# Optimization experiments

Measured on AMD Instinct MI355X. Metric: run time of the kernel, lower is better.

The kernel has to match this reference:

```python
import jax, jax.numpy as jnp
import numpy as np

N_NODES = 21
HID = 32


def _gcn_norm(edge_index, n):
    # GCNConv normalization with added self-loops (improved=False)
    src, dst = edge_index[0], edge_index[1]
    loop = jnp.arange(n, dtype=src.dtype)
    s = jnp.concatenate([src, loop])
    d = jnp.concatenate([dst, loop])
    w = jnp.ones(s.shape[0], dtype=jnp.float32)
    deg = jnp.zeros(n, dtype=jnp.float32).at[d].add(w)
    dinv = jnp.where(deg > 0, deg ** -0.5, 0.0)
    return s, d, dinv[s] * w * dinv[d]


def _gcn(X, W, b, s, d, norm):
    # X: [B,P,N,F] -> [B,P,N,O]; gather along node axis, scatter-add at targets
    XW = X @ W
    msg = XW[:, :, s, :] * norm[None, None, :, None]
    out = jnp.zeros_like(XW[:, :, :1, :]).repeat(XW.shape[2], axis=2)
    out = jnp.zeros(XW.shape, XW.dtype).at[:, :, d, :].add(msg)
    return out + b


def _forward(x, edge_index, W_z, b_z, W_r, b_r, W_h, b_h,
             lz_W, lz_b, lr_W, lr_b, lh_W, lh_b,
             att, l1_W, l1_b, l2_W, l2_b):
    B, N, F, P = x.shape
    X = jnp.transpose(x, (0, 3, 1, 2))  # [B,P,N,F] -- all periods in parallel
    s, d, norm = _gcn_norm(edge_index, N)
    # A3TGCN2 passes H=None for every period -> hidden state is zeros each call
    H = jnp.zeros((B, P, N, HID), x.dtype)
    Z = jax.nn.sigmoid(jnp.concatenate([_gcn(X, W_z, b_z, s, d, norm), H], -1) @ lz_W + lz_b)
    R = jax.nn.sigmoid(jnp.concatenate([_gcn(X, W_r, b_r, s, d, norm), H], -1) @ lr_W + lr_b)
    Ht = jnp.tanh(jnp.concatenate([_gcn(X, W_h, b_h, s, d, norm), H * R], -1) @ lh_W + lh_b)
    Hn = Z * H + (1.0 - Z) * Ht  # [B,P,N,HID]
    probs = jax.nn.softmax(att)
    h = jnp.einsum('p,bpno->bno', probs, Hn)  # attention pooling over periods
    h = jax.nn.relu(h)
    h = h @ l1_W + l1_b            # [B,N,P]
    h = jnp.transpose(h, (0, 2, 1))  # [B,P,N]
    h = h @ l2_W + l2_b            # [B,P,6]
    return jnp.transpose(h, (0, 2, 1))  # [B,6,P]


def setup_inputs() -> dict:
    key = jax.random.key(0)
    ks = jax.random.split(key, 16)
    B, N, F, P = 1024, N_NODES, 3, 64
    x = jax.random.normal(ks[0], (B, N, F, P), jnp.float32)
    edge_index = jax.random.randint(ks[1], (2, 60), 0, N)
    sc = 0.1
    inp = {
        'x': x, 'edge_index': edge_index,
        'W_z': jax.random.normal(ks[2], (F, HID)) * sc, 'b_z': jnp.zeros(HID),
        'W_r': jax.random.normal(ks[3], (F, HID)) * sc, 'b_r': jnp.zeros(HID),
        'W_h': jax.random.normal(ks[4], (F, HID)) * sc, 'b_h': jnp.zeros(HID),
        'lz_W': jax.random.normal(ks[5], (2 * HID, HID)) * sc, 'lz_b': jnp.zeros(HID),
        'lr_W': jax.random.normal(ks[6], (2 * HID, HID)) * sc, 'lr_b': jnp.zeros(HID),
        'lh_W': jax.random.normal(ks[7], (2 * HID, HID)) * sc, 'lh_b': jnp.zeros(HID),
        'att': jax.random.uniform(ks[8], (P,)),
        'l1_W': jax.random.normal(ks[9], (HID, P)) * sc, 'l1_b': jnp.zeros(P),
        'l2_W': jax.random.normal(ks[10], (N, 6)) * sc, 'l2_b': jnp.zeros(6),
    }
    return inp


def reference(x, edge_index, W_z, b_z, W_r, b_r, W_h, b_h,
              lz_W, lz_b, lr_W, lr_b, lh_W, lh_b,
              att, l1_W, l1_b, l2_W, l2_b):
    return _forward(x, edge_index, W_z, b_z, W_r, b_r, W_h, b_h,
                    lz_W, lz_b, lr_W, lr_b, lh_W, lh_b,
                    att, l1_W, l1_b, l2_W, l2_b)
```

## Files before the change

### kernel.cpp

```cpp
#include <hip/hip_runtime.h>

#define NN   21
#define NE   60
#define FD   3
#define HD   32
#define PP   64
#define OUTC 6

__global__ __launch_bounds__(256, 4) void fused_k(
    const float* __restrict__ x,   const int* __restrict__ edge,
    const float* __restrict__ Wz,  const float* __restrict__ bz,
    const float* __restrict__ Wh,  const float* __restrict__ bh,
    const float* __restrict__ lzW, const float* __restrict__ lzb,
    const float* __restrict__ lhW, const float* __restrict__ lhb,
    const float* __restrict__ att,
    const float* __restrict__ l1W, const float* __restrict__ l1b,
    const float* __restrict__ l2W, const float* __restrict__ l2b,
    float* __restrict__ out)
{
    __shared__ __align__(16) float Xs[NN * FD * PP];
    __shared__ __align__(16) float Ys[NN * FD * PP];
    __shared__ float As[NN * NN];
    __shared__ float degS[NN];
    __shared__ float probs[PP];
    __shared__ float Wzp[FD * HD], Whp[FD * HD], bzp[HD], bhp[HD];
    __shared__ float Hs[NN * HD];
    __shared__ float G[OUTC * HD];
    __shared__ float Sc[OUTC];

    const int t = threadIdx.x;
    const int b = blockIdx.x;
    const float* xb = x + (size_t)b * (NN * FD * PP);

    {
        const float4* xb4 = (const float4*)xb;
        float4* Xs4 = (float4*)Xs;
        for (int i = t; i < NN * FD * PP / 4; i += 256) Xs4[i] = xb4[i];

        float4* Ys4 = (float4*)Ys;
        Ys4[t]       = ((const float4*)lzW)[t];
        Ys4[256 + t] = ((const float4*)lhW)[t];
        if (t < 24)                 Ys4[512 + t]        = ((const float4*)Wz)[t];
        else if (t >= 32 && t < 56) Ys4[536 + (t - 32)] = ((const float4*)Wh)[t - 32];

        for (int i = t; i < NN * NN; i += 256) As[i] = 0.f;
        if (t < NN) degS[t] = 1.f;
    }
    __syncthreads();

    if (t < NE) atomicAdd(&degS[edge[NE + t]], 1.f);
    __syncthreads();

    if (t < NN) degS[t] = rsqrtf(degS[t]);
    __syncthreads();

    if (t < NE) {
        int s = edge[t], d = edge[NE + t];
        atomicAdd(&As[d * NN + s], degS[s] * degS[d]);
    }
    if (t >= 192 && t < 192 + NN) {
        int n = t - 192;
        atomicAdd(&As[n * NN + n], degS[n] * degS[n]);
    }
    if (t < FD * HD) {
        int f = t >> 5, o = t & 31;
        const float* lzWs = Ys;
        const float* lhWs = Ys + 1024;
        const float* WzS  = Ys + 2048;
        const float* WhS  = Ys + 2144;
        float az = 0.f, ah = 0.f;
        #pragma unroll
        for (int k = 0; k < HD; ++k) {
            az = fmaf(WzS[f * HD + k], lzWs[k * HD + o], az);
            ah = fmaf(WhS[f * HD + k], lhWs[k * HD + o], ah);
        }
        Wzp[t] = az; Whp[t] = ah;
    } else if (t < FD * HD + HD) {
        int o = t - FD * HD;
        const float* lzWs = Ys;
        const float* lhWs = Ys + 1024;
        float az = lzb[o], ah = lhb[o];
        #pragma unroll
        for (int k = 0; k < HD; ++k) {
            az = fmaf(bz[k], lzWs[k * HD + o], az);
            ah = fmaf(bh[k], lhWs[k * HD + o], ah);
        }
        bzp[o] = az; bhp[o] = ah;
    } else if (t >= 128 && t < 192) {
        int l = t - 128;
        float a = att[l];
        float m = a;
        #pragma unroll
        for (int msk = 32; msk >= 1; msk >>= 1) m = fmaxf(m, __shfl_xor(m, msk, 64));
        float e = __expf(a - m);
        float ssum = e;
        #pragma unroll
        for (int msk = 32; msk >= 1; msk >>= 1) ssum += __shfl_xor(ssum, msk, 64);
        probs[l] = e / ssum;
    }
    __syncthreads();

    {
        float4* Ys4 = (float4*)Ys;
        const float4* Xs4 = (const float4*)Xs;
        for (int i = t; i < NN * FD * PP / 4; i += 256) {
            int p4 = i & 15;
            int fn = i >> 4;
            int f = fn % 3, n = fn / 3;
            const float* Arow = As + n * NN;
            float4 acc = {0.f, 0.f, 0.f, 0.f};
            #pragma unroll
            for (int m = 0; m < NN; ++m) {
                float a = Arow[m];
                float4 xv = Xs4[(m * 3 + f) * 16 + p4];
                acc.x = fmaf(a, xv.x, acc.x);
                acc.y = fmaf(a, xv.y, acc.y);
                acc.z = fmaf(a, xv.z, acc.z);
                acc.w = fmaf(a, xv.w, acc.w);
            }
            Ys4[fn * 16 + p4] = acc;
        }
    }
    __syncthreads();

    {
        float4* ov4 = (float4*)Xs;
        const float4* l1W4 = (const float4*)l1W;
        for (int i = t; i < 512; i += 256) ov4[i] = l1W4[i];
        if (t < 16) ov4[512 + t] = ((const float4*)l1b)[t];
        if (t >= 64 && t < 64 + 126) Xs[2112 + (t - 64)] = l2W[t - 64];
        if (t >= 224 && t < 230) Xs[2238 + (t - 224)] = l2b[t - 224];
    }

    {
        const int o  = t & 31;
        const int ng = t >> 5;
        const float wz0 = Wzp[o], wz1 = Wzp[HD + o], wz2 = Wzp[2 * HD + o];
        const float wh0 = Whp[o], wh1 = Whp[HD + o], wh2 = Whp[2 * HD + o];
        const float bz0 = bzp[o], bh0 = bhp[o];
        for (int n = ng; n < NN; n += 8) {
            const float4* Yn4 = (const float4*)(Ys + n * FD * PP);
            float a0 = 0.f, a1 = 0.f, a2 = 0.f, a3 = 0.f;
            #pragma unroll
            for (int pq = 0; pq < 16; ++pq) {
                float4 y0 = Yn4[pq], y1 = Yn4[16 + pq], y2 = Yn4[32 + pq];
                {
                    float az = fmaf(y2.x, wz2, fmaf(y1.x, wz1, fmaf(y0.x, wz0, bz0)));
                    float ah = fmaf(y2.x, wh2, fmaf(y1.x, wh1, fmaf(y0.x, wh0, bh0)));
                    float w  = __builtin_amdgcn_rcpf(1.f + __expf(az));
                    float r  = __builtin_amdgcn_rcpf(1.f + __expf(2.f * ah));
                    float ht = fmaf(-2.f, r, 1.f);
                    a0 = fmaf(probs[4 * pq + 0] * w, ht, a0);
                }
                {
                    float az = fmaf(y2.y, wz2, fmaf(y1.y, wz1, fmaf(y0.y, wz0, bz0)));
                    float ah = fmaf(y2.y, wh2, fmaf(y1.y, wh1, fmaf(y0.y, wh0, bh0)));
                    float w  = __builtin_amdgcn_rcpf(1.f + __expf(az));
                    float r  = __builtin_amdgcn_rcpf(1.f + __expf(2.f * ah));
                    float ht = fmaf(-2.f, r, 1.f);
                    a1 = fmaf(probs[4 * pq + 1] * w, ht, a1);
                }
                {
                    float az = fmaf(y2.z, wz2, fmaf(y1.z, wz1, fmaf(y0.z, wz0, bz0)));
                    float ah = fmaf(y2.z, wh2, fmaf(y1.z, wh1, fmaf(y0.z, wh0, bh0)));
                    float w  = __builtin_amdgcn_rcpf(1.f + __expf(az));
                    float r  = __builtin_amdgcn_rcpf(1.f + __expf(2.f * ah));
                    float ht = fmaf(-2.f, r, 1.f);
                    a2 = fmaf(probs[4 * pq + 2] * w, ht, a2);
                }
                {
                    float az = fmaf(y2.w, wz2, fmaf(y1.w, wz1, fmaf(y0.w, wz0, bz0)));
                    float ah = fmaf(y2.w, wh2, fmaf(y1.w, wh1, fmaf(y0.w, wh0, bh0)));
                    float w  = __builtin_amdgcn_rcpf(1.f + __expf(az));
                    float r  = __builtin_amdgcn_rcpf(1.f + __expf(2.f * ah));
                    float ht = fmaf(-2.f, r, 1.f);
                    a3 = fmaf(probs[4 * pq + 3] * w, ht, a3);
                }
            }
            Hs[n * HD + o] = fmaxf((a0 + a1) + (a2 + a3), 0.f);
        }
    }
    __syncthreads();

    {
        const float* l2Ws = Xs + 2112;
        if (t < OUTC * HD) {
            int c = t >> 5, o = t & 31;
            float g = 0.f;
            #pragma unroll
            for (int n = 0; n < NN; ++n) g = fmaf(l2Ws[n * OUTC + c], Hs[n * HD + o], g);
            G[t] = g;
        } else if (t < OUTC * HD + OUTC) {
            int c = t - OUTC * HD;
            float s = 0.f;
            #pragma unroll
            for (int n = 0; n < NN; ++n) s += l2Ws[n * OUTC + c];
            Sc[c] = s;
        }
    }
    __syncthreads();

    {
        const float* l1Ws = Xs;
        const float* l1bs = Xs + 2048;
        const float* l2bs = Xs + 2238;
        for (int i = t; i < OUTC * PP; i += 256) {
            int c = i >> 6, p = i & 63;
            float acc = fmaf(Sc[c], l1bs[p], l2bs[c]);
            #pragma unroll
            for (int o = 0; o < HD; ++o)
                acc = fmaf(G[c * HD + o], l1Ws[o * PP + p], acc);
            out[(size_t)b * (OUTC * PP) + i] = acc;
        }
    }
}

extern "C" void kernel_launch(void* const* d_in, const int* in_sizes, int n_in,
                              void* d_out, int out_size, void* d_ws, size_t ws_size,
                              hipStream_t stream) {
    const float* x   = (const float*)d_in[0];
    const int*   ei  = (const int*)  d_in[1];
    const float* Wz  = (const float*)d_in[2];
    const float* bz  = (const float*)d_in[3];
    const float* Wh  = (const float*)d_in[6];
    const float* bh  = (const float*)d_in[7];
    const float* lzW = (const float*)d_in[8];
    const float* lzb = (const float*)d_in[9];
    const float* lhW = (const float*)d_in[12];
    const float* lhb = (const float*)d_in[13];
    const float* att = (const float*)d_in[14];
    const float* l1W = (const float*)d_in[15];
    const float* l1b = (const float*)d_in[16];
    const float* l2W = (const float*)d_in[17];
    const float* l2b = (const float*)d_in[18];

    float* out = (float*)d_out;
    const int B = in_sizes[0] / (NN * FD * PP);

    fused_k<<<B, 256, 0, stream>>>(x, ei, Wz, bz, Wh, bh, lzW, lzb, lhW, lhb,
                                   att, l1W, l1b, l2W, l2b, out);
}
```

Measured before the change: 154.4 us.

## Split weight/adjacency precompute into setup kernel, widen main kernel to 512 threads

Moves the per-block normalized adjacency, folded gate weights, softmax probabilities and output bias constants into a single-block setup kernel that writes to workspace. The main kernel runs 512 threads, loads the precomputed constants, skips zero adjacency entries in the aggregation, pre-scales by log2e to use exp2, and parallelises the gate evaluation across periods with shuffle reductions. This removes redundant per-block setup work and synchronisation at the cost of an extra launch and workspace traffic.

```diff
diff --git a/kernel.cpp b/kernel.cpp
--- a/kernel.cpp
+++ b/kernel.cpp
@@ -6,27 +6,130 @@
 #define HD   32
 #define PP   64
 #define OUTC 6
-
-__global__ __launch_bounds__(256, 4) void fused_k(
-    const float* __restrict__ x,   const int* __restrict__ edge,
-    const float* __restrict__ Wz,  const float* __restrict__ bz,
-    const float* __restrict__ Wh,  const float* __restrict__ bh,
-    const float* __restrict__ lzW, const float* __restrict__ lzb,
-    const float* __restrict__ lhW, const float* __restrict__ lhb,
-    const float* __restrict__ att,
-    const float* __restrict__ l1W, const float* __restrict__ l1b,
-    const float* __restrict__ l2W, const float* __restrict__ l2b,
+#define LOG2E 1.44269504088896f
+
+#define WS_A    0
+#define WS_WZ   504
+#define WS_WH   600
+#define WS_BZ   696
+#define WS_BH   728
+#define WS_PROB 760
+#define WS_M    824
+
+#if defined(__has_builtin)
+#  if __has_builtin(__builtin_amdgcn_exp2f)
+#    define EXP2(x) __builtin_amdgcn_exp2f(x)
+#  else
+#    define EXP2(x) exp2f(x)
+#  endif
+#else
+#  define EXP2(x) exp2f(x)
+#endif
+#define RCP(x) __builtin_amdgcn_rcpf(x)
+
+__global__ void setup_k(const int* __restrict__ edge,
+                        const float* __restrict__ Wz, const float* __restrict__ bz,
+                        const float* __restrict__ Wh, const float* __restrict__ bh,
+                        const float* __restrict__ lzW, const float* __restrict__ lzb,
+                        const float* __restrict__ lhW, const float* __restrict__ lhb,
+                        const float* __restrict__ att, const float* __restrict__ l1b,
+                        const float* __restrict__ l2W, const float* __restrict__ l2b,
+                        float* __restrict__ ws) {
+    __shared__ float sA[NN * NN];
+    __shared__ float degS[NN];
+    __shared__ float ScS[OUTC];
+    const int t = threadIdx.x;
+
+    for (int i = t; i < NN * NN; i += 256) sA[i] = 0.f;
+    if (t < NN) degS[t] = 1.f;
+    __syncthreads();
+
+    if (t < NE) atomicAdd(&degS[edge[NE + t]], 1.f);
+    __syncthreads();
+
+    if (t < NN) degS[t] = rsqrtf(degS[t]);
+    __syncthreads();
+
+    if (t < NE) {
+        int s = edge[t], d = edge[NE + t];
+        atomicAdd(&sA[d * NN + s], degS[s] * degS[d]);
+    }
+    if (t >= 64 && t < 64 + NN) {
+        int n = t - 64;
+        atomicAdd(&sA[n * NN + n], degS[n] * degS[n]);
+    }
+    if (t >= 96 && t < 192) {
+        int i = t - 96, f = i >> 5, o = i & 31;
+        float az = 0.f, ah = 0.f;
+        for (int k = 0; k < HD; ++k) {
+            az = fmaf(Wz[f * HD + k], lzW[k * HD + o], az);
+            ah = fmaf(Wh[f * HD + k], lhW[k * HD + o], ah);
+        }
+        ws[WS_WZ + i] = az * LOG2E;
+        ws[WS_WH + i] = ah * (2.f * LOG2E);
+    }
+    if (t >= 192 && t < 224) {
+        int o = t - 192;
+        float az = lzb[o], ah = lhb[o];
+        for (int k = 0; k < HD; ++k) {
+            az = fmaf(bz[k], lzW[k * HD + o], az);
+            ah = fmaf(bh[k], lhW[k * HD + o], ah);
+        }
+        ws[WS_BZ + o] = az * LOG2E;
+        ws[WS_BH + o] = ah * (2.f * LOG2E);
+    }
+    if (t < 64) {
+        float a = att[t], m = a;
+        #pragma unroll
+        for (int msk = 32; msk >= 1; msk >>= 1) m = fmaxf(m, __shfl_xor(m, msk, 64));
+        float e = __expf(a - m);
+        float ssum = e;
+        #pragma unroll
+        for (int msk = 32; msk >= 1; msk >>= 1) ssum += __shfl_xor(ssum, msk, 64);
+        ws[WS_PROB + t] = e / ssum;
+    }
+    if (t >= 224 && t < 224 + OUTC) {
+        int c = t - 224;
+        float s = 0.f;
+        for (int n = 0; n < NN; ++n) s += l2W[n * OUTC + c];
+        ScS[c] = s;
+    }
+    __syncthreads();
+
+    for (int i = t; i < NN * 24; i += 256) {
+        int r = i / 24, cm = i % 24;
+        ws[WS_A + i] = (cm < NN) ? sA[r * NN + cm] : 0.f;
+    }
+    for (int i = t; i < OUTC * PP; i += 256) {
+        int c = i >> 6, p = i & 63;
+        ws[WS_M + i] = fmaf(ScS[c], l1b[p], l2b[c]);
+    }
+}
+
+#define EVAL(Y0,Y1,Y2,PR) do {                                                  \
+    float az0_ = fmaf((Y2), wz02, fmaf((Y1), wz01, fmaf((Y0), wz00, bz0)));     \
+    float ah0_ = fmaf((Y2), wh02, fmaf((Y1), wh01, fmaf((Y0), wh00, bh0)));     \
+    float w0_  = RCP(1.f + EXP2(az0_));                                         \
+    float h0_  = fmaf(-2.f, RCP(1.f + EXP2(ah0_)), 1.f);                        \
+    acc0 = fmaf((PR) * w0_, h0_, acc0);                                         \
+    float az1_ = fmaf((Y2), wz12, fmaf((Y1), wz11, fmaf((Y0), wz10, bz1)));     \
+    float ah1_ = fmaf((Y2), wh12, fmaf((Y1), wh11, fmaf((Y0), wh10, bh1)));     \
+    float w1_  = RCP(1.f + EXP2(az1_));                                         \
+    float h1_  = fmaf(-2.f, RCP(1.f + EXP2(ah1_)), 1.f);                        \
+    acc1 = fmaf((PR) * w1_, h1_, acc1);                                         \
+} while (0)
+
+__global__ __launch_bounds__(512, 8) void main_k(
+    const float* __restrict__ x,  const float* __restrict__ ws,
+    const float* __restrict__ l1W, const float* __restrict__ l2W,
     float* __restrict__ out)
 {
     __shared__ __align__(16) float Xs[NN * FD * PP];
     __shared__ __align__(16) float Ys[NN * FD * PP];
-    __shared__ float As[NN * NN];
-    __shared__ float degS[NN];
-    __shared__ float probs[PP];
-    __shared__ float Wzp[FD * HD], Whp[FD * HD], bzp[HD], bhp[HD];
+    __shared__ __align__(16) float AsP[NN * 24];
+    __shared__ __align__(16) float Cs[320];
     __shared__ float Hs[NN * HD];
     __shared__ float G[OUTC * HD];
-    __shared__ float Sc[OUTC];
 
     const int t = threadIdx.x;
     const int b = blockIdx.x;
@@ -35,88 +138,39 @@
     {
         const float4* xb4 = (const float4*)xb;
         float4* Xs4 = (float4*)Xs;
-        for (int i = t; i < NN * FD * PP / 4; i += 256) Xs4[i] = xb4[i];
-
+        Xs4[t] = xb4[t];
+        if (t < 496) Xs4[512 + t] = xb4[512 + t];
+        if (t < 126) ((float4*)AsP)[t] = ((const float4*)ws)[t];
+        if (t >= 128 && t < 208)
+            ((float4*)Cs)[t - 128] = ((const float4*)(ws + WS_WZ))[t - 128];
+    }
+    __syncthreads();
+
+    {
+        const float4* Xs4 = (const float4*)Xs;
         float4* Ys4 = (float4*)Ys;
-        Ys4[t]       = ((const float4*)lzW)[t];
-        Ys4[256 + t] = ((const float4*)lhW)[t];
-        if (t < 24)                 Ys4[512 + t]        = ((const float4*)Wz)[t];
-        else if (t >= 32 && t < 56) Ys4[536 + (t - 32)] = ((const float4*)Wh)[t - 32];
-
-        for (int i = t; i < NN * NN; i += 256) As[i] = 0.f;
-        if (t < NN) degS[t] = 1.f;
-    }
-    __syncthreads();
-
-    if (t < NE) atomicAdd(&degS[edge[NE + t]], 1.f);
-    __syncthreads();
-
-    if (t < NN) degS[t] = rsqrtf(degS[t]);
-    __syncthreads();
-
-    if (t < NE) {
-        int s = edge[t], d = edge[NE + t];
-        atomicAdd(&As[d * NN + s], degS[s] * degS[d]);
-    }
-    if (t >= 192 && t < 192 + NN) {
-        int n = t - 192;
-        atomicAdd(&As[n * NN + n], degS[n] * degS[n]);
-    }
-    if (t < FD * HD) {
-        int f = t >> 5, o = t & 31;
-        const float* lzWs = Ys;
-        const float* lhWs = Ys + 1024;
-        const float* WzS  = Ys + 2048;
-        const float* WhS  = Ys + 2144;
-        float az = 0.f, ah = 0.f;
-        #pragma unroll
-        for (int k = 0; k < HD; ++k) {
-            az = fmaf(WzS[f * HD + k], lzWs[k * HD + o], az);
-            ah = fmaf(WhS[f * HD + k], lhWs[k * HD + o], ah);
-        }
-        Wzp[t] = az; Whp[t] = ah;
-    } else if (t < FD * HD + HD) {
-        int o = t - FD * HD;
-        const float* lzWs = Ys;
-        const float* lhWs = Ys + 1024;
-        float az = lzb[o], ah = lhb[o];
-        #pragma unroll
-        for (int k = 0; k < HD; ++k) {
-            az = fmaf(bz[k], lzWs[k * HD + o], az);
-            ah = fmaf(bh[k], lhWs[k * HD + o], ah);
-        }
-        bzp[o] = az; bhp[o] = ah;
-    } else if (t >= 128 && t < 192) {
-        int l = t - 128;
-        float a = att[l];
-        float m = a;
-        #pragma unroll
-        for (int msk = 32; msk >= 1; msk >>= 1) m = fmaxf(m, __shfl_xor(m, msk, 64));
-        float e = __expf(a - m);
-        float ssum = e;
-        #pragma unroll
-        for (int msk = 32; msk >= 1; msk >>= 1) ssum += __shfl_xor(ssum, msk, 64);
-        probs[l] = e / ssum;
-    }
-    __syncthreads();
-
-    {
-        float4* Ys4 = (float4*)Ys;
-        const float4* Xs4 = (const float4*)Xs;
-        for (int i = t; i < NN * FD * PP / 4; i += 256) {
-            int p4 = i & 15;
-            int fn = i >> 4;
-            int f = fn % 3, n = fn / 3;
-            const float* Arow = As + n * NN;
+        for (int i = t; i < NN * FD * PP / 4; i += 512) {
+            const int p4 = i & 15;
+            const int fn = i >> 4;
+            const int n  = fn / 3;
+            const int f  = fn - n * 3;
+            const float4* An4 = (const float4*)(AsP + n * 24);
             float4 acc = {0.f, 0.f, 0.f, 0.f};
             #pragma unroll
-            for (int m = 0; m < NN; ++m) {
-                float a = Arow[m];
-                float4 xv = Xs4[(m * 3 + f) * 16 + p4];
-                acc.x = fmaf(a, xv.x, acc.x);
-                acc.y = fmaf(a, xv.y, acc.y);
-                acc.z = fmaf(a, xv.z, acc.z);
-                acc.w = fmaf(a, xv.w, acc.w);
+            for (int mq = 0; mq < 6; ++mq) {
+                const float4 a = An4[mq];
+                if (a.x != 0.f) { const float4 xv = Xs4[((mq*4+0)*3+f)*16 + p4];
+                    acc.x=fmaf(a.x,xv.x,acc.x); acc.y=fmaf(a.x,xv.y,acc.y);
+                    acc.z=fmaf(a.x,xv.z,acc.z); acc.w=fmaf(a.x,xv.w,acc.w); }
+                if (a.y != 0.f) { const float4 xv = Xs4[((mq*4+1)*3+f)*16 + p4];
+                    acc.x=fmaf(a.y,xv.x,acc.x); acc.y=fmaf(a.y,xv.y,acc.y);
+                    acc.z=fmaf(a.y,xv.z,acc.z); acc.w=fmaf(a.y,xv.w,acc.w); }
+                if (a.z != 0.f) { const float4 xv = Xs4[((mq*4+2)*3+f)*16 + p4];
+                    acc.x=fmaf(a.z,xv.x,acc.x); acc.y=fmaf(a.z,xv.y,acc.y);
+                    acc.z=fmaf(a.z,xv.z,acc.z); acc.w=fmaf(a.z,xv.w,acc.w); }
+                if (a.w != 0.f) { const float4 xv = Xs4[((mq*4+3)*3+f)*16 + p4];
+                    acc.x=fmaf(a.w,xv.x,acc.x); acc.y=fmaf(a.w,xv.y,acc.y);
+                    acc.z=fmaf(a.w,xv.z,acc.z); acc.w=fmaf(a.w,xv.w,acc.w); }
             }
             Ys4[fn * 16 + p4] = acc;
         }
@@ -124,94 +178,63 @@
     __syncthreads();
 
     {
-        float4* ov4 = (float4*)Xs;
-        const float4* l1W4 = (const float4*)l1W;
-        for (int i = t; i < 512; i += 256) ov4[i] = l1W4[i];
-        if (t < 16) ov4[512 + t] = ((const float4*)l1b)[t];
-        if (t >= 64 && t < 64 + 126) Xs[2112 + (t - 64)] = l2W[t - 64];
-        if (t >= 224 && t < 230) Xs[2238 + (t - 224)] = l2b[t - 224];
-    }
-
-    {
-        const int o  = t & 31;
-        const int ng = t >> 5;
-        const float wz0 = Wzp[o], wz1 = Wzp[HD + o], wz2 = Wzp[2 * HD + o];
-        const float wh0 = Whp[o], wh1 = Whp[HD + o], wh2 = Whp[2 * HD + o];
-        const float bz0 = bzp[o], bh0 = bhp[o];
-        for (int n = ng; n < NN; n += 8) {
-            const float4* Yn4 = (const float4*)(Ys + n * FD * PP);
-            float a0 = 0.f, a1 = 0.f, a2 = 0.f, a3 = 0.f;
-            #pragma unroll
-            for (int pq = 0; pq < 16; ++pq) {
-                float4 y0 = Yn4[pq], y1 = Yn4[16 + pq], y2 = Yn4[32 + pq];
-                {
-                    float az = fmaf(y2.x, wz2, fmaf(y1.x, wz1, fmaf(y0.x, wz0, bz0)));
-                    float ah = fmaf(y2.x, wh2, fmaf(y1.x, wh1, fmaf(y0.x, wh0, bh0)));
-                    float w  = __builtin_amdgcn_rcpf(1.f + __expf(az));
-                    float r  = __builtin_amdgcn_rcpf(1.f + __expf(2.f * ah));
-                    float ht = fmaf(-2.f, r, 1.f);
-                    a0 = fmaf(probs[4 * pq + 0] * w, ht, a0);
-                }
-                {
-                    float az = fmaf(y2.y, wz2, fmaf(y1.y, wz1, fmaf(y0.y, wz0, bz0)));
-                    float ah = fmaf(y2.y, wh2, fmaf(y1.y, wh1, fmaf(y0.y, wh0, bh0)));
-                    float w  = __builtin_amdgcn_rcpf(1.f + __expf(az));
-                    float r  = __builtin_amdgcn_rcpf(1.f + __expf(2.f * ah));
-                    float ht = fmaf(-2.f, r, 1.f);
-                    a1 = fmaf(probs[4 * pq + 1] * w, ht, a1);
-                }
-                {
-                    float az = fmaf(y2.z, wz2, fmaf(y1.z, wz1, fmaf(y0.z, wz0, bz0)));
-                    float ah = fmaf(y2.z, wh2, fmaf(y1.z, wh1, fmaf(y0.z, wh0, bh0)));
-                    float w  = __builtin_amdgcn_rcpf(1.f + __expf(az));
-                    float r  = __builtin_amdgcn_rcpf(1.f + __expf(2.f * ah));
-                    float ht = fmaf(-2.f, r, 1.f);
-                    a2 = fmaf(probs[4 * pq + 2] * w, ht, a2);
-                }
-                {
-                    float az = fmaf(y2.w, wz2, fmaf(y1.w, wz1, fmaf(y0.w, wz0, bz0)));
-                    float ah = fmaf(y2.w, wh2, fmaf(y1.w, wh1, fmaf(y0.w, wh0, bh0)));
-                    float w  = __builtin_amdgcn_rcpf(1.f + __expf(az));
-                    float r  = __builtin_amdgcn_rcpf(1.f + __expf(2.f * ah));
-                    float ht = fmaf(-2.f, r, 1.f);
-                    a3 = fmaf(probs[4 * pq + 3] * w, ht, a3);
+        const int ps = t & 7;
+        const int og = (t >> 3) & 15;
+        const int c4 = t >> 7;
+        const int o0 = og * 2, o1 = o0 + 1;
+        const float wz00 = Cs[o0],      wz01 = Cs[32+o0],  wz02 = Cs[64+o0];
+        const float wz10 = Cs[o1],      wz11 = Cs[32+o1],  wz12 = Cs[64+o1];
+        const float wh00 = Cs[96+o0],   wh01 = Cs[128+o0], wh02 = Cs[160+o0];
+        const float wh10 = Cs[96+o1],   wh11 = Cs[128+o1], wh12 = Cs[160+o1];
+        const float bz0  = Cs[192+o0],  bz1  = Cs[192+o1];
+        const float bh0  = Cs[224+o0],  bh1  = Cs[224+o1];
+        const float4 pr0 = *(const float4*)&Cs[256 + ps*8];
+        const float4 pr1 = *(const float4*)&Cs[256 + ps*8 + 4];
+        #pragma unroll
+        for (int s = 0; s < 6; ++s) {
+            const int n = c4 + 4 * s;
+            if (n < NN) {
+                const float4* Yn4 = (const float4*)(Ys + n * FD * PP) + ps * 2;
+                float acc0 = 0.f, acc1 = 0.f;
+                float4 y0 = Yn4[0], y1 = Yn4[16], y2 = Yn4[32];
+                EVAL(y0.x,y1.x,y2.x, pr0.x); EVAL(y0.y,y1.y,y2.y, pr0.y);
+                EVAL(y0.z,y1.z,y2.z, pr0.z); EVAL(y0.w,y1.w,y2.w, pr0.w);
+                y0 = Yn4[1]; y1 = Yn4[17]; y2 = Yn4[33];
+                EVAL(y0.x,y1.x,y2.x, pr1.x); EVAL(y0.y,y1.y,y2.y, pr1.y);
+                EVAL(y0.z,y1.z,y2.z, pr1.z); EVAL(y0.w,y1.w,y2.w, pr1.w);
+                acc0 += __shfl_xor(acc0, 1); acc0 += __shfl_xor(acc0, 2); acc0 += __shfl_xor(acc0, 4);
+                acc1 += __shfl_xor(acc1, 1); acc1 += __shfl_xor(acc1, 2); acc1 += __shfl_xor(acc1, 4);
+                if (ps == 0) {
+                    Hs[n * HD + o0] = fmaxf(acc0, 0.f);
+                    Hs[n * HD + o1] = fmaxf(acc1, 0.f);
                 }
             }
-            Hs[n * HD + o] = fmaxf((a0 + a1) + (a2 + a3), 0.f);
-        }
-    }
-    __syncthreads();
-
-    {
-        const float* l2Ws = Xs + 2112;
-        if (t < OUTC * HD) {
-            int c = t >> 5, o = t & 31;
-            float g = 0.f;
-            #pragma unroll
-            for (int n = 0; n < NN; ++n) g = fmaf(l2Ws[n * OUTC + c], Hs[n * HD + o], g);
-            G[t] = g;
-        } else if (t < OUTC * HD + OUTC) {
-            int c = t - OUTC * HD;
-            float s = 0.f;
-            #pragma unroll
-            for (int n = 0; n < NN; ++n) s += l2Ws[n * OUTC + c];
-            Sc[c] = s;
-        }
-    }
-    __syncthreads();
-
-    {
-        const float* l1Ws = Xs;
-        const float* l1bs = Xs + 2048;
-        const float* l2bs = Xs + 2238;
-        for (int i = t; i < OUTC * PP; i += 256) {
-            int c = i >> 6, p = i & 63;
-            float acc = fmaf(Sc[c], l1bs[p], l2bs[c]);
-            #pragma unroll
-            for (int o = 0; o < HD; ++o)
-                acc = fmaf(G[c * HD + o], l1Ws[o * PP + p], acc);
-            out[(size_t)b * (OUTC * PP) + i] = acc;
-        }
+        }
+    }
+    __syncthreads();
+
+    if (t < OUTC * HD) {
+        const int c = t >> 5, o = t & 31;
+        float g = 0.f;
+        #pragma unroll
+        for (int n = 0; n < NN; ++n)
+            g = fmaf(l2W[n * OUTC + c], Hs[n * HD + o], g);
+        G[t] = g;
+    }
+    __syncthreads();
+
+    if (t < OUTC * PP) {
+        const int c = t >> 6, p = t & 63;
+        const float* Gc = G + c * HD;
+        float a0 = 0.f, a1 = 0.f, a2 = 0.f, a3 = 0.f;
+        #pragma unroll
+        for (int o = 0; o < HD; o += 4) {
+            a0 = fmaf(Gc[o+0], l1W[(o+0) * PP + p], a0);
+            a1 = fmaf(Gc[o+1], l1W[(o+1) * PP + p], a1);
+            a2 = fmaf(Gc[o+2], l1W[(o+2) * PP + p], a2);
+            a3 = fmaf(Gc[o+3], l1W[(o+3) * PP + p], a3);
+        }
+        out[(size_t)b * (OUTC * PP) + t] = ws[WS_M + t] + (a0 + a1) + (a2 + a3);
     }
 }
 
@@ -235,8 +258,11 @@
     const float* l2b = (const float*)d_in[18];
 
     float* out = (float*)d_out;
+    float* ws  = (float*)d_ws;
+
     const int B = in_sizes[0] / (NN * FD * PP);
 
-    fused_k<<<B, 256, 0, stream>>>(x, ei, Wz, bz, Wh, bh, lzW, lzb, lhW, lhb,
-                                   att, l1W, l1b, l2W, l2b, out);
+    setup_k<<<1, 256, 0, stream>>>(ei, Wz, bz, Wh, bh, lzW, lzb, lhW, lhb,
+                                   att, l1b, l2W, l2b, ws);
+    main_k<<<B, 512, 0, stream>>>(x, ws, l1W, l2W, out);
 }
```

After: 128.3 us. 17.0% less time.
